# Kernel tuning notes

Measured on AMD Instinct MI355X. Metric: run time of the kernel, lower is better.

## Reference

```python
import jax, jax.numpy as jnp
import numpy as np

B, C1, C2, H, L, D, NC = 32, 256, 256, 64, 40, 768, 8
SIGMA_W = 0.1
EMB = (D + NC * 2) // 2  # 392


def _conv(x, w, scale, shift, pad):
    # ultralytics-style Conv: conv2d(bias=False) + eval-mode BN (folded into per-channel
    # scale/shift) + SiLU activation
    y = jax.lax.conv_general_dilated(x, w, (1, 1), [(pad, pad), (pad, pad)],
                                     dimension_numbers=('NCHW', 'OIHW', 'NCHW'))
    y = y * scale[None, :, None, None] + shift[None, :, None, None]
    return y * jax.nn.sigmoid(y)  # SiLU


def _l2norm(x, eps=1e-12):
    n = jnp.sqrt(jnp.sum(x * x, axis=1, keepdims=True))
    return x / jnp.maximum(n, eps)


def setup_inputs() -> dict:
    key = jax.random.key(0)
    ks = jax.random.split(key, 20)
    img = jax.random.normal(ks[0], (B, C1, H, H), jnp.float32)
    flang = jax.random.normal(ks[1], (B, L, D), jnp.float32)
    # contiguous valid mask with >=3 tokens (CLS + >=1 word + SEP)
    lens = jax.random.randint(ks[2], (B,), 3, L + 1)
    word_mask = (jnp.arange(L)[None, :] < lens[:, None]).astype(jnp.int32)
    p = lambda k, s: jax.random.normal(k, s, jnp.float32) * 0.02
    return {
        'img': img, 'flang': flang, 'word_mask': word_mask,
        'w_visu': p(ks[3], (C2, C1, 1, 1)), 's_visu': jnp.ones((C2,)), 'b_visu': jnp.zeros((C2,)),
        'w_g': p(ks[4], (NC, NC, 1, 1)), 's_g': jnp.ones((NC,)), 'b_g': jnp.zeros((NC,)),
        'w_b': p(ks[5], (NC, NC, 1, 1)), 's_b': jnp.ones((NC,)), 'b_b': jnp.zeros((NC,)),
        'W1': p(ks[6], (EMB, D)), 'b1': jnp.zeros((EMB,)),
        'W2': p(ks[7], (2 * NC, EMB)), 'b2': jnp.zeros((2 * NC,)),
        'w_f1': p(ks[8], (C1, C1, 1, 1)), 's_f1': jnp.ones((C1,)), 'b_f1': jnp.zeros((C1,)),
        'w_f2': p(ks[9], (C1, C1, 3, 3)), 's_f2': jnp.ones((C1,)), 'b_f2': jnp.zeros((C1,)),
        'w_f3': p(ks[10], (C2, C1, 1, 1)), 'bias_f3': jnp.zeros((C2,)),
        'add_weight': jnp.zeros((), jnp.float32),
    }


def reference(img, flang, word_mask, w_visu, s_visu, b_visu, w_g, s_g, b_g,
              w_b, s_b, b_b, W1, b1, W2, b2, w_f1, s_f1, b_f1, w_f2, s_f2, b_f2,
              w_f3, bias_f3, add_weight):
    height = img.shape[2]
    # mapping_visu: Conv 1x1 + BN + SiLU, then tanh
    map_visu = jnp.tanh(_conv(img, w_visu, s_visu, b_visu, 0))  # [B,C2,H,H]

    # vectorized get_avg_flang: mean over selected tokens excluding first and last selected
    m = word_mask.astype(jnp.int32)
    csum = jnp.cumsum(m, axis=1)                     # [B,L]
    total = csum[:, -1:]
    inner = ((m == 1) & (csum > 1) & (csum < total)).astype(flang.dtype)  # [B,L]
    cnt = jnp.sum(inner, axis=1, keepdims=True)
    flang_avg = jnp.sum(flang * inner[:, :, None], axis=1) / cnt  # [B,D]

    # mapping_lang: two stacked Linears (no activation between), then sigmoid
    h = flang_avg @ W1.T + b1
    map_flang = jax.nn.sigmoid(h @ W2.T + b2)        # [B,2*NC]
    maps = map_flang.reshape(-1, NC, 2)

    sigma = SIGMA_W * height
    yc = (maps[:, :, 0] * height).astype(jnp.int32)[:, :, None, None]
    xc = (maps[:, :, 1] * height).astype(jnp.int32)[:, :, None, None]
    gy, gx = jnp.meshgrid(jnp.arange(height), jnp.arange(height), indexing='ij')
    gy = gy[None, None]; gx = gx[None, None]
    d2 = ((gy - yc) ** 2 + (gx - xc) ** 2).astype(jnp.float32)
    weights = jnp.exp(-d2 / (2.0 * sigma ** 2))      # [B,NC,H,H]

    gamma = jnp.tanh(_conv(weights, w_g, s_g, b_g, 0))
    beta = jnp.tanh(_conv(weights, w_b, s_b, b_b, 0))
    g = jnp.mean(gamma, axis=1, keepdims=True)       # [B,1,H,H]
    b = jnp.max(beta, axis=1, keepdims=True)         # [B,1,H,H]

    v_film = _l2norm(g * map_visu + b)               # [B,C2,H,H]
    # mapping_fusion: Conv1x1 -> Conv3x3 -> plain Conv2d 1x1 with bias
    v = _conv(v_film, w_f1, s_f1, b_f1, 0)
    v = _conv(v, w_f2, s_f2, b_f2, 1)
    v_film = jax.lax.conv_general_dilated(v, w_f3, (1, 1), [(0, 0), (0, 0)],
                                          dimension_numbers=('NCHW', 'OIHW', 'NCHW'))
    v_film = v_film + bias_f3[None, :, None, None]

    add_w = jnp.tanh(add_weight)
    v_add = (1.0 + add_w) * img + (1.0 - add_w) * v_film
    return _l2norm(v_add)
```

## Files before the change

kernel.cpp:

```cpp
#include <hip/hip_runtime.h>
#include <hip/hip_bf16.h>

#define B_   32
#define C_   256
#define HH   64
#define P_   4096
#define L_   40
#define D_   768
#define NC_  8
#define EMB_ 392
#define CP_  (C_*P_)
#define LOS  264

typedef __attribute__((ext_vector_type(8))) short bf16x8;
typedef __attribute__((ext_vector_type(4))) float f32x4;
typedef unsigned short u16;

static __device__ __forceinline__ float silu_fast(float y) {
    return __fdividef(y, 1.f + __expf(-y));
}
static __device__ __forceinline__ float tanh_fast(float x) {
    return 1.f - __fdividef(2.f, __expf(2.f * x) + 1.f);
}
static __device__ __forceinline__ u16 f2b(float f) {
    __hip_bfloat16 h = __float2bfloat16(f);
    return *reinterpret_cast<u16*>(&h);
}
static __device__ __forceinline__ float b2f(u16 u) {
    unsigned v = ((unsigned)u) << 16;
    return __int_as_float((int)v);
}

typedef __attribute__((address_space(1))) const unsigned int g_u32;
typedef __attribute__((address_space(3))) unsigned int l_u32;
static __device__ __forceinline__ void gl_lds(const u16* g, short* l) {
    __builtin_amdgcn_global_load_lds((g_u32*)g, (l_u32*)l, 16, 0, 0);
}
#define VMCNT6() asm volatile("s_waitcnt vmcnt(6)" ::: "memory")
#define VMCNT0() asm volatile("s_waitcnt vmcnt(0)" ::: "memory")
#define RBAR()  do { __builtin_amdgcn_s_barrier(); __builtin_amdgcn_sched_barrier(0); } while (0)

__global__ __launch_bounds__(256) void k_prep(
    const float* __restrict__ wv, const float* __restrict__ wf1,
    const float* __restrict__ wf3, const float* __restrict__ wf2,
    u16* __restrict__ WV, u16* __restrict__ WF1,
    u16* __restrict__ WF3, u16* __restrict__ WF2, u16* __restrict__ zbig)
{
    int i = blockIdx.x * 256 + threadIdx.x;
    int oc = i >> 8, ic = i & 255;
    WV[i]  = f2b(wv[i]);
    WF1[i] = f2b(wf1[i]);
    WF3[i] = f2b(wf3[i]);
#pragma unroll
    for (int tap = 0; tap < 9; ++tap)
        WF2[oc * 2304 + tap * 256 + ic] = f2b(wf2[oc * 2304 + ic * 9 + tap]);
    if (blockIdx.x == 0) {
        for (int z = threadIdx.x; z < 1024; z += 256) zbig[z] = 0;
    }
}

__global__ __launch_bounds__(256) void k_imgT(
    const float* __restrict__ img, u16* __restrict__ imgT)
{
    int b = blockIdx.z, pix0 = blockIdx.x * 32, ic0 = blockIdx.y * 32;
    int t = threadIdx.x;
    __shared__ float T[32][33];
    int ic = t >> 3, ps = (t & 7) * 4;
    f32x4 v = *(const f32x4*)&img[((size_t)b * C_ + ic0 + ic) * P_ + pix0 + ps];
    T[ic][ps] = v[0]; T[ic][ps + 1] = v[1]; T[ic][ps + 2] = v[2]; T[ic][ps + 3] = v[3];
    __syncthreads();
    int px = t >> 3, sg = (t & 7) * 4;
    u16 o0 = f2b(T[sg + 0][px]), o1 = f2b(T[sg + 1][px]);
    u16 o2 = f2b(T[sg + 2][px]), o3 = f2b(T[sg + 3][px]);
    uint2 val;
    val.x = (unsigned)o0 | ((unsigned)o1 << 16);
    val.y = (unsigned)o2 | ((unsigned)o3 << 16);
    *(uint2*)(imgT + ((size_t)b * P_ + pix0 + px) * C_ + ic0 + sg) = val;
}

__global__ __launch_bounds__(256) void k_lang(
    const float* __restrict__ flang, const int* __restrict__ wmask,
    const float* __restrict__ W1, const float* __restrict__ b1,
    const float* __restrict__ W2, const float* __restrict__ b2,
    int* __restrict__ centers)
{
    int b = blockIdx.x, tid = threadIdx.x;
    __shared__ float inner[L_];
    __shared__ float cnt_s;
    __shared__ float favg[D_];
    __shared__ float hbuf[EMB_];
    __shared__ float mfs[16];

    if (tid == 0) {
        int total = 0;
        for (int l = 0; l < L_; ++l) total += wmask[b * L_ + l];
        int c = 0, cntv = 0;
        for (int l = 0; l < L_; ++l) {
            int m = wmask[b * L_ + l];
            c += m;
            float f = (m == 1 && c > 1 && c < total) ? 1.f : 0.f;
            inner[l] = f;
            cntv += (f != 0.f);
        }
        cnt_s = (float)cntv;
    }
    __syncthreads();
    float cinv = 1.f / cnt_s;
    for (int d = tid; d < D_; d += 256) {
        float s = 0.f;
        for (int l = 0; l < L_; ++l)
            s += flang[((size_t)b * L_ + l) * D_ + d] * inner[l];
        favg[d] = s * cinv;
    }
    __syncthreads();
    for (int e = tid; e < EMB_; e += 256) {
        float s = b1[e];
        const float* w = W1 + (size_t)e * D_;
        for (int d = 0; d < D_; ++d) s += w[d] * favg[d];
        hbuf[e] = s;
    }
    __syncthreads();
    if (tid < 16) {
        float s = b2[tid];
        const float* w = W2 + tid * EMB_;
        for (int d = 0; d < EMB_; ++d) s += w[d] * hbuf[d];
        mfs[tid] = 1.f / (1.f + expf(-s));
    }
    __syncthreads();
    if (tid < NC_) {
        centers[b * (NC_ * 2) + tid * 2 + 0] = (int)(mfs[tid * 2 + 0] * (float)HH);
        centers[b * (NC_ * 2) + tid * 2 + 1] = (int)(mfs[tid * 2 + 1] * (float)HH);
    }
}

__global__ __launch_bounds__(256) void k_gb(
    const int* __restrict__ centers,
    const float* __restrict__ wg, const float* __restrict__ sg, const float* __restrict__ bg,
    const float* __restrict__ wb, const float* __restrict__ sb, const float* __restrict__ bb,
    float* __restrict__ gmap, float* __restrict__ bmap)
{
    int idx = blockIdx.x * 256 + threadIdx.x;
    int b = idx >> 12;
    int p = idx & 4095;
    int gy = p >> 6, gx = p & 63;

    float w[NC_];
#pragma unroll
    for (int nc = 0; nc < NC_; ++nc) {
        int yc = centers[b * (NC_ * 2) + nc * 2 + 0];
        int xc = centers[b * (NC_ * 2) + nc * 2 + 1];
        int dy = gy - yc, dx = gx - xc;
        w[nc] = __expf(-(float)(dy * dy + dx * dx) / 81.92f);
    }
    float gsum = 0.f, bmx = -1e30f;
#pragma unroll
    for (int c = 0; c < NC_; ++c) {
        float ag = 0.f, ab = 0.f;
#pragma unroll
        for (int ic = 0; ic < NC_; ++ic) {
            ag += wg[c * NC_ + ic] * w[ic];
            ab += wb[c * NC_ + ic] * w[ic];
        }
        gsum += tanh_fast(silu_fast(sg[c] * ag + bg[c]));
        bmx = fmaxf(bmx, tanh_fast(silu_fast(sb[c] * ab + bb[c])));
    }
    gmap[idx] = gsum * (1.f / (float)NC_);
    bmap[idx] = bmx;
}

static __device__ __forceinline__ void frag_load(const short* sA, const short* sW,
                                                 int l15, int qa, int w,
                                                 bf16x8 a[8], bf16x8 bb[4])
{
#pragma unroll
    for (int m = 0; m < 8; ++m)
        a[m] = *(const bf16x8*)&sA[(m * 16 + l15) * 32 + qa * 8];
#pragma unroll
    for (int n = 0; n < 4; ++n)
        bb[n] = *(const bf16x8*)&sW[(w * 64 + n * 16 + l15) * 32 + qa * 8];
}
static __device__ __forceinline__ void frag_compute(const bf16x8 a[8], const bf16x8 bb[4],
                                                    f32x4 acc[8][4])
{
#pragma unroll
    for (int m = 0; m < 8; ++m)
#pragma unroll
        for (int n = 0; n < 4; ++n)
            acc[m][n] = __builtin_amdgcn_mfma_f32_16x16x32_bf16(a[m], bb[n], acc[m][n], 0, 0, 0);
}

__global__ __launch_bounds__(256, 2) void k_visu(
    const u16* __restrict__ X, const u16* __restrict__ W,
    const float* __restrict__ s_visu, const float* __restrict__ b_visu,
    const float* __restrict__ gmap, const float* __restrict__ bmap,
    u16* __restrict__ Y)
{
    int b = blockIdx.y, p0 = blockIdx.x * 128, t = threadIdx.x;
    int lane = t & 63, w = t >> 6;
    int l15 = t & 15, q = (t >> 4) & 3;
    int qa = q ^ ((l15 >> 1) & 3);
    int lc = (lane & 3) ^ ((lane >> 3) & 3);
    int lp = lane >> 2;
    __shared__ __align__(16) short SM[3 * 12288];
    __shared__ float red[4][128];
    __shared__ float invs[128];
    const u16* Xb = X + (size_t)b * CP_;

    f32x4 acc[8][4];
#pragma unroll
    for (int m = 0; m < 8; ++m)
#pragma unroll
        for (int n = 0; n < 4; ++n) acc[m][n] = (f32x4)0.f;

    auto stage = [&](int s, int buf) {
        int k0 = s * 32;
        short* bA = SM + buf * 12288;
        short* bW = bA + 4096;
#pragma unroll
        for (int i = 0; i < 2; ++i) {
            int pr = (w * 2 + i) * 16 + lp;
            gl_lds(Xb + (size_t)(p0 + pr) * C_ + k0 + lc * 8, bA + (w * 2 + i) * 512);
        }
#pragma unroll
        for (int j = 0; j < 4; ++j) {
            int oc = (w * 4 + j) * 16 + lp;
            gl_lds(W + (size_t)oc * 256 + k0 + lc * 8, bW + (w * 4 + j) * 512);
        }
    };

    stage(0, 0);
    stage(1, 1);
    VMCNT6();
    RBAR();
    int cur = 0;
    for (int s = 0; s < 8; ++s) {
        const short* bA = SM + cur * 12288;
        bf16x8 a[8], bb[4];
        frag_load(bA, bA + 4096, l15, qa, w, a, bb);
        if (s < 6) stage(s + 2, (cur == 0) ? 2 : cur - 1);
        frag_compute(a, bb, acc);
        if (s < 6) { VMCNT6(); } else { VMCNT0(); }
        RBAR();
        cur = (cur == 2) ? 0 : cur + 1;
    }

    float sc[4], sh[4];
#pragma unroll
    for (int n = 0; n < 4; ++n) {
        int oc = w * 64 + n * 16 + l15;
        sc[n] = s_visu[oc]; sh[n] = b_visu[oc];
    }
    short* LO = SM;
#pragma unroll
    for (int m = 0; m < 8; ++m) {
        f32x4 gv = *(const f32x4*)&gmap[(size_t)b * P_ + p0 + m * 16 + q * 4];
        f32x4 bm = *(const f32x4*)&bmap[(size_t)b * P_ + p0 + m * 16 + q * 4];
        float ps[4] = {0.f, 0.f, 0.f, 0.f};
#pragma unroll
        for (int n = 0; n < 4; ++n)
#pragma unroll
            for (int r = 0; r < 4; ++r) {
                float y = sc[n] * acc[m][n][r] + sh[n];
                float v = gv[r] * tanh_fast(silu_fast(y)) + bm[r];
                ps[r] += v * v;
                LO[(m * 16 + q * 4 + r) * LOS + w * 64 + n * 16 + l15] = (short)f2b(v);
            }
#pragma unroll
        for (int r = 0; r < 4; ++r) {
            float p = ps[r];
            p += __shfl_xor(p, 1);
            p += __shfl_xor(p, 2);
            p += __shfl_xor(p, 4);
            p += __shfl_xor(p, 8);
            if (l15 == 0) red[w][m * 16 + q * 4 + r] = p;
        }
    }
    __syncthreads();
    if (t < 128) {
        float s = red[0][t] + red[1][t] + red[2][t] + red[3][t];
        invs[t] = 1.f / fmaxf(sqrtf(s), 1e-12f);
    }
    __syncthreads();

    u16* Yb = Y + (size_t)b * CP_ + (size_t)p0 * C_;
#pragma unroll
    for (int h = 0; h < 2; ++h) {
        int row = h * 64 + (t >> 2);
        float inv = invs[row];
        const short* sp = &LO[row * LOS];
        u16* dp = Yb + (size_t)row * C_;
#pragma unroll
        for (int u = 0; u < 8; ++u) {
            int c = (t & 3) * 8 + u * 32;
            uint4 vv = *(const uint4*)(sp + c);
            const u16* e = (const u16*)&vv;
            uint4 o;
            u16* oe = (u16*)&o;
#pragma unroll
            for (int k = 0; k < 8; ++k) oe[k] = f2b(b2f(e[k]) * inv);
            *(uint4*)(dp + c) = o;
        }
    }
}

__global__ __launch_bounds__(256, 2) void k_f1(
    const u16* __restrict__ X, const u16* __restrict__ W,
    const float* __restrict__ scale, const float* __restrict__ shift,
    u16* __restrict__ Y)
{
    int b = blockIdx.y, p0 = blockIdx.x * 128, t = threadIdx.x;
    int lane = t & 63, w = t >> 6;
    int l15 = t & 15, q = (t >> 4) & 3;
    int qa = q ^ ((l15 >> 1) & 3);
    int lc = (lane & 3) ^ ((lane >> 3) & 3);
    int lp = lane >> 2;
    __shared__ __align__(16) short SM[3 * 12288];
    const u16* Xb = X + (size_t)b * CP_;

    f32x4 acc[8][4];
#pragma unroll
    for (int m = 0; m < 8; ++m)
#pragma unroll
        for (int n = 0; n < 4; ++n) acc[m][n] = (f32x4)0.f;

    auto stage = [&](int s, int buf) {
        int k0 = s * 32;
        short* bA = SM + buf * 12288;
        short* bW = bA + 4096;
#pragma unroll
        for (int i = 0; i < 2; ++i) {
            int pr = (w * 2 + i) * 16 + lp;
            gl_lds(Xb + (size_t)(p0 + pr) * C_ + k0 + lc * 8, bA + (w * 2 + i) * 512);
        }
#pragma unroll
        for (int j = 0; j < 4; ++j) {
            int oc = (w * 4 + j) * 16 + lp;
            gl_lds(W + (size_t)oc * 256 + k0 + lc * 8, bW + (w * 4 + j) * 512);
        }
    };

    stage(0, 0);
    stage(1, 1);
    VMCNT6();
    RBAR();
    int cur = 0;
    for (int s = 0; s < 8; ++s) {
        const short* bA = SM + cur * 12288;
        bf16x8 a[8], bb[4];
        frag_load(bA, bA + 4096, l15, qa, w, a, bb);
        if (s < 6) stage(s + 2, (cur == 0) ? 2 : cur - 1);
        frag_compute(a, bb, acc);
        if (s < 6) { VMCNT6(); } else { VMCNT0(); }
        RBAR();
        cur = (cur == 2) ? 0 : cur + 1;
    }

    float sc[4], sh[4];
#pragma unroll
    for (int n = 0; n < 4; ++n) {
        int oc = w * 64 + n * 16 + l15;
        sc[n] = scale[oc]; sh[n] = shift[oc];
    }
    short* LO = SM;
#pragma unroll
    for (int m = 0; m < 8; ++m)
#pragma unroll
        for (int n = 0; n < 4; ++n)
#pragma unroll
            for (int r = 0; r < 4; ++r) {
                float v = silu_fast(sc[n] * acc[m][n][r] + sh[n]);
                LO[(m * 16 + q * 4 + r) * LOS + w * 64 + n * 16 + l15] = (short)f2b(v);
            }
    __syncthreads();

    u16* Yb = Y + (size_t)b * CP_ + (size_t)p0 * C_;
#pragma unroll
    for (int h = 0; h < 2; ++h) {
        int row = h * 64 + (t >> 2);
        const short* sp = &LO[row * LOS];
        u16* dp = Yb + (size_t)row * C_;
#pragma unroll
        for (int u = 0; u < 8; ++u) {
            int c = (t & 3) * 8 + u * 32;
            *(uint4*)(dp + c) = *(const uint4*)(sp + c);
        }
    }
}

__global__ __launch_bounds__(256, 2) void k_f2(
    const u16* __restrict__ X, const u16* __restrict__ W,
    const float* __restrict__ scale, const float* __restrict__ shift,
    const u16* __restrict__ zbig, u16* __restrict__ Y)
{
    int b = blockIdx.y, p0 = blockIdx.x * 128, t = threadIdx.x;
    int lane = t & 63, w = t >> 6;
    int l15 = t & 15, q = (t >> 4) & 3;
    int qa = q ^ ((l15 >> 1) & 3);
    int lc = (lane & 3) ^ ((lane >> 3) & 3);
    int lp = lane >> 2;
    __shared__ __align__(16) short SM[3 * 12288];
    const u16* Xb = X + (size_t)b * CP_;

    f32x4 acc[8][4];
#pragma unroll
    for (int m = 0; m < 8; ++m)
#pragma unroll
        for (int n = 0; n < 4; ++n) acc[m][n] = (f32x4)0.f;

    const u16* ap0 = zbig;
    const u16* ap1 = zbig;
    const u16* wp0 = W + (size_t)((w * 4 + 0) * 16 + lp) * 2304 + lc * 8;
    const u16* wp1 = W + (size_t)((w * 4 + 1) * 16 + lp) * 2304 + lc * 8;
    const u16* wp2 = W + (size_t)((w * 4 + 2) * 16 + lp) * 2304 + lc * 8;
    const u16* wp3 = W + (size_t)((w * 4 + 3) * 16 + lp) * 2304 + lc * 8;
    int ss = 0;

    auto stage_next = [&](int buf) {
        if ((ss & 7) == 0) {
            int tap = ss >> 3;
            int dy = tap / 3 - 1, dx = tap - (tap / 3) * 3 - 1;
            int pA = p0 + (w * 2 + 0) * 16 + lp;
            int y0 = (pA >> 6) + dy, x0 = (pA & 63) + dx;
            ap0 = ((unsigned)y0 < (unsigned)HH && (unsigned)x0 < (unsigned)HH)
                  ? Xb + (size_t)(y0 * HH + x0) * C_ + lc * 8 : zbig + lc * 8;
            int pB = p0 + (w * 2 + 1) * 16 + lp;
            int y1 = (pB >> 6) + dy, x1 = (pB & 63) + dx;
            ap1 = ((unsigned)y1 < (unsigned)HH && (unsigned)x1 < (unsigned)HH)
                  ? Xb + (size_t)(y1 * HH + x1) * C_ + lc * 8 : zbig + lc * 8;
        }
        short* bA = SM + buf * 12288;
        short* bW = bA + 4096;
        gl_lds(ap0, bA + (w * 2 + 0) * 512);
        gl_lds(ap1, bA + (w * 2 + 1) * 512);
        gl_lds(wp0, bW + (w * 4 + 0) * 512);
        gl_lds(wp1, bW + (w * 4 + 1) * 512);
        gl_lds(wp2, bW + (w * 4 + 2) * 512);
        gl_lds(wp3, bW + (w * 4 + 3) * 512);
        ap0 += 32; ap1 += 32;
        wp0 += 32; wp1 += 32; wp2 += 32; wp3 += 32;
        ++ss;
    };

    stage_next(0);
    stage_next(1);
    VMCNT6();
    RBAR();
    int cur = 0;
    for (int s = 0; s < 72; ++s) {
        const short* bA = SM + cur * 12288;
        bf16x8 a[8], bb[4];
        frag_load(bA, bA + 4096, l15, qa, w, a, bb);
        if (s < 70) {
            int nb = cur == 0 ? 2 : cur - 1;
            stage_next(nb);
        }
        frag_compute(a, bb, acc);
        if (s < 70) { VMCNT6(); } else { VMCNT0(); }
        RBAR();
        cur = cur == 2 ? 0 : cur + 1;
    }

    float sc[4], sh[4];
#pragma unroll
    for (int n = 0; n < 4; ++n) {
        int oc = w * 64 + n * 16 + l15;
        sc[n] = scale[oc]; sh[n] = shift[oc];
    }
    short* LO = SM;
#pragma unroll
    for (int m = 0; m < 8; ++m)
#pragma unroll
        for (int n = 0; n < 4; ++n)
#pragma unroll
            for (int r = 0; r < 4; ++r) {
                float v = silu_fast(sc[n] * acc[m][n][r] + sh[n]);
                LO[(m * 16 + q * 4 + r) * LOS + w * 64 + n * 16 + l15] = (short)f2b(v);
            }
    __syncthreads();

    u16* Yb = Y + (size_t)b * CP_ + (size_t)p0 * C_;
#pragma unroll
    for (int h = 0; h < 2; ++h) {
        int row = h * 64 + (t >> 2);
        const short* sp = &LO[row * LOS];
        u16* dp = Yb + (size_t)row * C_;
#pragma unroll
        for (int u = 0; u < 8; ++u) {
            int c = (t & 3) * 8 + u * 32;
            *(uint4*)(dp + c) = *(const uint4*)(sp + c);
        }
    }
}

__global__ __launch_bounds__(256, 2) void k_final(
    const u16* __restrict__ X, const u16* __restrict__ W,
    const float* __restrict__ bias_f3, const float* __restrict__ img,
    const float* __restrict__ add_w, float* __restrict__ out)
{
    int b = blockIdx.y, p0 = blockIdx.x * 128, t = threadIdx.x;
    int lane = t & 63, w = t >> 6;
    int l15 = t & 15, q = (t >> 4) & 3;
    int qa = q ^ ((l15 >> 1) & 3);
    int lc = (lane & 3) ^ ((lane >> 3) & 3);
    int lp = lane >> 2;
    __shared__ __align__(16) short SM[3 * 12288];
    __shared__ float red[4][128];
    __shared__ float invs[128];
    const u16* Xb = X + (size_t)b * CP_;

    f32x4 acc[8][4];
#pragma unroll
    for (int m = 0; m < 8; ++m)
#pragma unroll
        for (int n = 0; n < 4; ++n) acc[m][n] = (f32x4)0.f;

    auto stage = [&](int s, int buf) {
        int k0 = s * 32;
        short* bA = SM + buf * 12288;
        short* bW = bA + 4096;
#pragma unroll
        for (int i = 0; i < 2; ++i) {
            int pr = (w * 2 + i) * 16 + lp;
            gl_lds(Xb + (size_t)(p0 + pr) * C_ + k0 + lc * 8, bA + (w * 2 + i) * 512);
        }
#pragma unroll
        for (int j = 0; j < 4; ++j) {
            int oc = (w * 4 + j) * 16 + lp;
            gl_lds(W + (size_t)oc * 256 + k0 + lc * 8, bW + (w * 4 + j) * 512);
        }
    };

    stage(0, 0);
    stage(1, 1);
    VMCNT6();
    RBAR();
    int cur = 0;
    for (int s = 0; s < 8; ++s) {
        const short* bA = SM + cur * 12288;
        bf16x8 a[8], bb[4];
        frag_load(bA, bA + 4096, l15, qa, w, a, bb);
        if (s < 6) stage(s + 2, (cur == 0) ? 2 : cur - 1);
        frag_compute(a, bb, acc);
        if (s < 6) { VMCNT6(); } else { VMCNT0(); }
        RBAR();
        cur = (cur == 2) ? 0 : cur + 1;
    }

    float aw = tanhf(add_w[0]);
    float c1 = 1.f + aw, c2 = 1.f - aw;
    float bf[4];
#pragma unroll
    for (int n = 0; n < 4; ++n) bf[n] = bias_f3[w * 64 + n * 16 + l15];

#pragma unroll
    for (int m = 0; m < 8; ++m) {
        float ps[4] = {0.f, 0.f, 0.f, 0.f};
#pragma unroll
        for (int n = 0; n < 4; ++n) {
            int oc = w * 64 + n * 16 + l15;
            f32x4 iv = *(const f32x4*)&img[((size_t)b * C_ + oc) * P_ + p0 + m * 16 + q * 4];
#pragma unroll
            for (int r = 0; r < 4; ++r) {
                float v = c1 * iv[r] + c2 * (acc[m][n][r] + bf[n]);
                acc[m][n][r] = v;
                ps[r] += v * v;
            }
        }
#pragma unroll
        for (int r = 0; r < 4; ++r) {
            float p = ps[r];
            p += __shfl_xor(p, 1);
            p += __shfl_xor(p, 2);
            p += __shfl_xor(p, 4);
            p += __shfl_xor(p, 8);
            if (l15 == 0) red[w][m * 16 + q * 4 + r] = p;
        }
    }
    __syncthreads();
    if (t < 128) {
        float s = red[0][t] + red[1][t] + red[2][t] + red[3][t];
        invs[t] = 1.f / fmaxf(sqrtf(s), 1e-12f);
    }
    __syncthreads();

    float* TP = (float*)SM;
#pragma unroll
    for (int cc = 0; cc < 2; ++cc) {
#pragma unroll
        for (int mm = 0; mm < 4; ++mm) {
            int m = cc * 4 + mm;
            f32x4 iv = *(const f32x4*)&invs[m * 16 + q * 4];
#pragma unroll
            for (int n = 0; n < 4; ++n) {
                int oc = w * 64 + n * 16 + l15;
                f32x4 o;
#pragma unroll
                for (int r = 0; r < 4; ++r) o[r] = acc[m][n][r] * iv[r];
                *(f32x4*)&TP[(size_t)oc * 68 + mm * 16 + q * 4] = o;
            }
        }
        __syncthreads();
        {
            int c16 = (t & 15) * 4;
#pragma unroll
            for (int u = 0; u < 16; ++u) {
                int row = u * 16 + (t >> 4);
                *(f32x4*)&out[((size_t)b * C_ + row) * P_ + p0 + cc * 64 + c16] =
                    *(const f32x4*)&TP[(size_t)row * 68 + c16];
            }
        }
        __syncthreads();
    }
}

extern "C" void kernel_launch(void* const* d_in, const int* in_sizes, int n_in,
                              void* d_out, int out_size, void* d_ws, size_t ws_size,
                              hipStream_t stream)
{
    const float* img     = (const float*)d_in[0];
    const float* flang   = (const float*)d_in[1];
    const int*   wmask   = (const int*)d_in[2];
    const float* w_visu  = (const float*)d_in[3];
    const float* s_visu  = (const float*)d_in[4];
    const float* b_visu  = (const float*)d_in[5];
    const float* w_g     = (const float*)d_in[6];
    const float* s_g     = (const float*)d_in[7];
    const float* b_g     = (const float*)d_in[8];
    const float* w_b     = (const float*)d_in[9];
    const float* s_b     = (const float*)d_in[10];
    const float* b_b     = (const float*)d_in[11];
    const float* W1      = (const float*)d_in[12];
    const float* b1      = (const float*)d_in[13];
    const float* W2      = (const float*)d_in[14];
    const float* b2      = (const float*)d_in[15];
    const float* w_f1    = (const float*)d_in[16];
    const float* s_f1    = (const float*)d_in[17];
    const float* b_f1    = (const float*)d_in[18];
    const float* w_f2    = (const float*)d_in[19];
    const float* s_f2    = (const float*)d_in[20];
    const float* b_f2    = (const float*)d_in[21];
    const float* w_f3    = (const float*)d_in[22];
    const float* bias_f3 = (const float*)d_in[23];
    const float* add_w   = (const float*)d_in[24];

    float* out = (float*)d_out;

    u16* bigA = (u16*)d_ws;
    u16* bigB = bigA + (size_t)B_ * CP_;
    u16* WV   = bigB + (size_t)B_ * CP_;
    u16* WF1  = WV + 65536;
    u16* WF3  = WF1 + 65536;
    u16* WF2  = WF3 + 65536;
    float* gmap = (float*)(WF2 + 589824);
    float* bmap = gmap + (size_t)B_ * P_;
    int* centers = (int*)(bmap + (size_t)B_ * P_);
    u16* zbig = (u16*)(centers + 512);

    k_prep<<<256, 256, 0, stream>>>(w_visu, w_f1, w_f3, w_f2, WV, WF1, WF3, WF2, zbig);
    k_lang<<<B_, 256, 0, stream>>>(flang, wmask, W1, b1, W2, b2, centers);
    k_gb<<<(B_ * P_) / 256, 256, 0, stream>>>(centers, w_g, s_g, b_g, w_b, s_b, b_b, gmap, bmap);
    k_imgT<<<dim3(P_ / 32, C_ / 32, B_), 256, 0, stream>>>(img, bigB);
    k_visu<<<dim3(P_ / 128, B_), 256, 0, stream>>>(bigB, WV, s_visu, b_visu, gmap, bmap, bigA);
    k_f1<<<dim3(P_ / 128, B_), 256, 0, stream>>>(bigA, WF1, s_f1, b_f1, bigB);
    k_f2<<<dim3(P_ / 128, B_), 256, 0, stream>>>(bigB, WF2, s_f2, b_f2, zbig, bigA);
    k_final<<<dim3(P_ / 128, B_), 256, 0, stream>>>(bigA, WF3, bias_f3, img, add_w, out);
}
```

Baseline: 443.5 us.

## Enlarge 3x3 conv tile to 256 pixels with 8 waves in 2x4 grid

The 3x3 fusion conv kernel now uses 512-thread blocks that each cover 256 pixels by 256 output channels. The 8 waves are laid out as 2 row groups by 4 column groups, so each weight tile staged in LDS is shared across twice as many pixels. This halves weight global loads per wave and lowers the pipeline wait count to match. In exchange it uses more LDS per block, allows only one block per CU, halves the grid size, and writes the epilogue out in two phases.

Measured after the change: 435.2 us, median of 3. Within noise of the previous version (-1.9%).

```diff
diff --git a/kernel.cpp b/kernel.cpp
--- a/kernel.cpp
+++ b/kernel.cpp
@@ -37,6 +37,7 @@
     __builtin_amdgcn_global_load_lds((g_u32*)g, (l_u32*)l, 16, 0, 0);
 }
 #define VMCNT6() asm volatile("s_waitcnt vmcnt(6)" ::: "memory")
+#define VMCNT4() asm volatile("s_waitcnt vmcnt(4)" ::: "memory")
 #define VMCNT0() asm volatile("s_waitcnt vmcnt(0)" ::: "memory")
 #define RBAR()  do { __builtin_amdgcn_s_barrier(); __builtin_amdgcn_sched_barrier(0); } while (0)
 
@@ -387,18 +388,19 @@
     }
 }
 
-__global__ __launch_bounds__(256, 2) void k_f2(
+__global__ __launch_bounds__(512, 1) void k_f2(
     const u16* __restrict__ X, const u16* __restrict__ W,
     const float* __restrict__ scale, const float* __restrict__ shift,
     const u16* __restrict__ zbig, u16* __restrict__ Y)
 {
-    int b = blockIdx.y, p0 = blockIdx.x * 128, t = threadIdx.x;
+    int b = blockIdx.y, p0 = blockIdx.x * 256, t = threadIdx.x;
     int lane = t & 63, w = t >> 6;
+    int wr = w >> 2, wc = w & 3;
     int l15 = t & 15, q = (t >> 4) & 3;
     int qa = q ^ ((l15 >> 1) & 3);
     int lc = (lane & 3) ^ ((lane >> 3) & 3);
     int lp = lane >> 2;
-    __shared__ __align__(16) short SM[3 * 12288];
+    __shared__ __align__(16) short SM[3 * 16384];
     const u16* Xb = X + (size_t)b * CP_;
 
     f32x4 acc[8][4];
@@ -409,10 +411,8 @@
 
     const u16* ap0 = zbig;
     const u16* ap1 = zbig;
-    const u16* wp0 = W + (size_t)((w * 4 + 0) * 16 + lp) * 2304 + lc * 8;
-    const u16* wp1 = W + (size_t)((w * 4 + 1) * 16 + lp) * 2304 + lc * 8;
-    const u16* wp2 = W + (size_t)((w * 4 + 2) * 16 + lp) * 2304 + lc * 8;
-    const u16* wp3 = W + (size_t)((w * 4 + 3) * 16 + lp) * 2304 + lc * 8;
+    const u16* wp0 = W + (size_t)((w * 2 + 0) * 16 + lp) * 2304 + lc * 8;
+    const u16* wp1 = W + (size_t)((w * 2 + 1) * 16 + lp) * 2304 + lc * 8;
     int ss = 0;
 
     auto stage_next = [&](int buf) {
@@ -428,34 +428,38 @@
             ap1 = ((unsigned)y1 < (unsigned)HH && (unsigned)x1 < (unsigned)HH)
                   ? Xb + (size_t)(y1 * HH + x1) * C_ + lc * 8 : zbig + lc * 8;
         }
-        short* bA = SM + buf * 12288;
-        short* bW = bA + 4096;
+        short* bA = SM + buf * 16384;
+        short* bW = bA + 8192;
         gl_lds(ap0, bA + (w * 2 + 0) * 512);
         gl_lds(ap1, bA + (w * 2 + 1) * 512);
-        gl_lds(wp0, bW + (w * 4 + 0) * 512);
-        gl_lds(wp1, bW + (w * 4 + 1) * 512);
-        gl_lds(wp2, bW + (w * 4 + 2) * 512);
-        gl_lds(wp3, bW + (w * 4 + 3) * 512);
+        gl_lds(wp0, bW + (w * 2 + 0) * 512);
+        gl_lds(wp1, bW + (w * 2 + 1) * 512);
         ap0 += 32; ap1 += 32;
-        wp0 += 32; wp1 += 32; wp2 += 32; wp3 += 32;
+        wp0 += 32; wp1 += 32;
         ++ss;
     };
 
     stage_next(0);
     stage_next(1);
-    VMCNT6();
+    VMCNT4();
     RBAR();
     int cur = 0;
     for (int s = 0; s < 72; ++s) {
-        const short* bA = SM + cur * 12288;
+        const short* bA = SM + cur * 16384;
+        const short* bW = bA + 8192;
         bf16x8 a[8], bb[4];
-        frag_load(bA, bA + 4096, l15, qa, w, a, bb);
+#pragma unroll
+        for (int m = 0; m < 8; ++m)
+            a[m] = *(const bf16x8*)&bA[(wr * 128 + m * 16 + l15) * 32 + qa * 8];
+#pragma unroll
+        for (int n = 0; n < 4; ++n)
+            bb[n] = *(const bf16x8*)&bW[(wc * 64 + n * 16 + l15) * 32 + qa * 8];
         if (s < 70) {
             int nb = cur == 0 ? 2 : cur - 1;
             stage_next(nb);
         }
         frag_compute(a, bb, acc);
-        if (s < 70) { VMCNT6(); } else { VMCNT0(); }
+        if (s < 70) { VMCNT4(); } else { VMCNT0(); }
         RBAR();
         cur = cur == 2 ? 0 : cur + 1;
     }
@@ -463,31 +467,36 @@
     float sc[4], sh[4];
 #pragma unroll
     for (int n = 0; n < 4; ++n) {
-        int oc = w * 64 + n * 16 + l15;
+        int oc = wc * 64 + n * 16 + l15;
         sc[n] = scale[oc]; sh[n] = shift[oc];
     }
     short* LO = SM;
-#pragma unroll
-    for (int m = 0; m < 8; ++m)
-#pragma unroll
-        for (int n = 0; n < 4; ++n)
-#pragma unroll
-            for (int r = 0; r < 4; ++r) {
-                float v = silu_fast(sc[n] * acc[m][n][r] + sh[n]);
-                LO[(m * 16 + q * 4 + r) * LOS + w * 64 + n * 16 + l15] = (short)f2b(v);
+    u16* Yb = Y + (size_t)b * CP_ + (size_t)p0 * C_;
+#pragma unroll
+    for (int h = 0; h < 2; ++h) {
+        __syncthreads();
+        if (wr == h) {
+#pragma unroll
+            for (int m = 0; m < 8; ++m)
+#pragma unroll
+                for (int n = 0; n < 4; ++n)
+#pragma unroll
+                    for (int r = 0; r < 4; ++r) {
+                        float v = silu_fast(sc[n] * acc[m][n][r] + sh[n]);
+                        LO[(m * 16 + q * 4 + r) * LOS + wc * 64 + n * 16 + l15] = (short)f2b(v);
+                    }
+        }
+        __syncthreads();
+        {
+            int row = t >> 2;
+            const short* sp = &LO[row * LOS];
+            u16* dp = Yb + (size_t)(h * 128 + row) * C_;
+#pragma unroll
+            for (int u = 0; u < 4; ++u) {
+                int c = (t & 3) * 8 + u * 64;
+                *(uint4*)(dp + c) = *(const uint4*)(sp + c);
+                *(uint4*)(dp + c + 32) = *(const uint4*)(sp + c + 32);
             }
-    __syncthreads();
-
-    u16* Yb = Y + (size_t)b * CP_ + (size_t)p0 * C_;
-#pragma unroll
-    for (int h = 0; h < 2; ++h) {
-        int row = h * 64 + (t >> 2);
-        const short* sp = &LO[row * LOS];
-        u16* dp = Yb + (size_t)row * C_;
-#pragma unroll
-        for (int u = 0; u < 8; ++u) {
-            int c = (t & 3) * 8 + u * 32;
-            *(uint4*)(dp + c) = *(const uint4*)(sp + c);
         }
     }
 }
@@ -662,6 +671,6 @@
     k_imgT<<<dim3(P_ / 32, C_ / 32, B_), 256, 0, stream>>>(img, bigB);
     k_visu<<<dim3(P_ / 128, B_), 256, 0, stream>>>(bigB, WV, s_visu, b_visu, gmap, bmap, bigA);
     k_f1<<<dim3(P_ / 128, B_), 256, 0, stream>>>(bigA, WF1, s_f1, b_f1, bigB);
-    k_f2<<<dim3(P_ / 128, B_), 256, 0, stream>>>(bigB, WF2, s_f2, b_f2, zbig, bigA);
+    k_f2<<<dim3(P_ / 256, B_), 512, 0, stream>>>(bigB, WF2, s_f2, b_f2, zbig, bigA);
     k_final<<<dim3(P_ / 128, B_), 256, 0, stream>>>(bigA, WF3, bias_f3, img, add_w, out);
 }
```
